# Kernel optimization log

Hardware: AMD Instinct MI355X
Metric: run time of the kernel (lower is better)

The kernel has to match this reference:

```python
import jax, jax.numpy as jnp
import numpy as np

NUM_HEADS = 16


def setup_inputs() -> dict:
    key = jax.random.key(0)
    ks = jax.random.split(key, 7)
    B, S, D = 2, 2048, 1024
    scale = 1.0 / np.sqrt(D)
    return {
        "queries": jax.random.normal(ks[0], (B, S, D), jnp.float32),
        "keys": jax.random.normal(ks[1], (B, S, D), jnp.float32),
        "values": jax.random.normal(ks[2], (B, S, D), jnp.float32),
        "Wq": jax.random.normal(ks[3], (D, D), jnp.float32) * scale,
        "Wk": jax.random.normal(ks[4], (D, D), jnp.float32) * scale,
        "Wv": jax.random.normal(ks[5], (D, D), jnp.float32) * scale,
        "Wo": jax.random.normal(ks[6], (D, D), jnp.float32) * scale,
    }


def _split_heads(x, h):
    # [B, S, D] -> [B, h, S, D/h]
    B, S, D = x.shape
    return x.reshape(B, S, h, D // h).transpose(0, 2, 1, 3)


def reference(queries, keys, values, Wq, Wk, Wv, Wo):
    h = NUM_HEADS
    q = _split_heads(queries @ Wq, h)  # [B, h, S, dh]
    k = _split_heads(keys @ Wk, h)
    v = _split_heads(values @ Wv, h)
    dh = q.shape[-1]
    scores = jnp.einsum("bhqd,bhkd->bhqk", q, k) / jnp.sqrt(jnp.float32(dh))
    attn = jax.nn.softmax(scores, axis=-1)
    y = jnp.einsum("bhqk,bhkd->bhqd", attn, v)  # [B, h, S, dh]
    B, _, S, _ = y.shape
    y = y.transpose(0, 2, 1, 3).reshape(B, S, h * dh)
    return y @ Wo
```

## Files before the change

### kernel.cpp

```cpp
#include <hip/hip_runtime.h>
#include <hip/hip_bf16.h>


typedef __attribute__((ext_vector_type(8))) short bf16x8;
typedef __attribute__((ext_vector_type(4))) float f32x4;
typedef __attribute__((ext_vector_type(16))) float f32x16;
typedef __attribute__((ext_vector_type(4))) unsigned int u32x4;

#define QSCALE 0.18033688011112042f

__device__ __forceinline__ unsigned short f2b(float f) {
    unsigned int u = __float_as_uint(f);
    u += 0x7FFFu + ((u >> 16) & 1u);
    return (unsigned short)(u >> 16);
}

__device__ __forceinline__ unsigned cvt_pk_bf16(float lo, float hi) {
    unsigned r;
    asm("v_cvt_pk_bf16_f32 %0, %1, %2" : "=v"(r) : "v"(lo), "v"(hi));
    return r;
}

__device__ __forceinline__ void gld_lds16(const void* g, void* l) {
    __builtin_amdgcn_global_load_lds(
        (const __attribute__((address_space(1))) unsigned int*)g,
        (__attribute__((address_space(3))) unsigned int*)l, 16, 0, 0);
}

__global__ __launch_bounds__(256) void f32_to_bf16_3(
    const float* __restrict__ i0, const float* __restrict__ i1, const float* __restrict__ i2,
    unsigned short* __restrict__ o0, unsigned short* __restrict__ o1, unsigned short* __restrict__ o2)
{
    const int z = blockIdx.y;
    const float* in = z == 0 ? i0 : (z == 1 ? i1 : i2);
    unsigned short* out = z == 0 ? o0 : (z == 1 ? o1 : o2);
    int i = blockIdx.x * 256 + threadIdx.x;
    float4 v = ((const float4*)in)[i];
    ushort4 o;
    o.x = f2b(v.x); o.y = f2b(v.y); o.z = f2b(v.z); o.w = f2b(v.w);
    ((ushort4*)out)[i] = o;
}

__global__ __launch_bounds__(256) void transpose_w4(
    const float* __restrict__ W0, const float* __restrict__ W1,
    const float* __restrict__ W2, const float* __restrict__ W3,
    unsigned short* __restrict__ O0, unsigned short* __restrict__ O1,
    unsigned short* __restrict__ O2, unsigned short* __restrict__ O3)
{
    __shared__ unsigned short tile[32][33];
    const int z = blockIdx.z;
    const float* in = z == 0 ? W0 : z == 1 ? W1 : z == 2 ? W2 : W3;
    unsigned short* out = z == 0 ? O0 : z == 1 ? O1 : z == 2 ? O2 : O3;
    const int c0 = blockIdx.x * 32, r0 = blockIdx.y * 32;
    const int tx = threadIdx.x, ty = threadIdx.y;
#pragma unroll
    for (int i = 0; i < 4; ++i)
        tile[ty + i * 8][tx] = f2b(in[(size_t)(r0 + ty + i * 8) * 1024 + c0 + tx]);
    __syncthreads();
#pragma unroll
    for (int i = 0; i < 4; ++i)
        out[(size_t)(c0 + ty + i * 8) * 1024 + r0 + tx] = tile[tx][ty + i * 8];
}

__device__ __forceinline__ void vpack_store(unsigned short* Vp, int gr, int gc,
                                            const f32x4& a)
{
    int bq = gr >> 11, kvg = gr & 2047, kvt = kvg >> 6;
    int h = gc >> 6, d = gc & 63;
    size_t img = ((size_t)(bq * 16 + h) * 32 + kvt) * 4096;
    int kvb = kvg & 63;
    int T = kvb >> 5, g = (kvb >> 3) & 3, hib = (kvb >> 2) & 1;
    int kstep = 2 * T + (g >> 1);
    int dt = d >> 5, ln31 = d & 31;
    size_t addr = img + dt * 2048 + kstep * 512 + hib * 256 + ln31 * 8 + (g & 1) * 4;
    uint2 w;
    w.x = cvt_pk_bf16(a[0], a[1]);
    w.y = cvt_pk_bf16(a[2], a[3]);
    *(uint2*)(Vp + addr) = w;
}

__device__ __forceinline__ void kpack_store(unsigned short* Kp, int gr0, int gc,
                                            const f32x4& a)
{
    int bq = gr0 >> 11, kvg = gr0 & 2047, kvt = kvg >> 6;
    int h = gc >> 6, d = gc & 63;
    size_t img = ((size_t)(bq * 16 + h) * 32 + kvt) * 4096;
    int ks = d >> 4, hib = (d >> 3) & 1, i = d & 7;
    int kvb = kvg & 63, T = kvb >> 5;
    size_t base = img + T * 2048 + ks * 512 + hib * 256 + i;
#pragma unroll
    for (int r = 0; r < 4; ++r)
        Kp[base + ((kvb & 31) + r) * 8] = f2b(a[r]);
}

__device__ __forceinline__ int lds_fragaddr(int slot, int mat, int half, int row,
                                            int ks, int lg)
{
    int c8s = lg ^ ((row >> 1) & 3);
    return slot * 32768 + mat * 16384 + half * 8192 +
           (((row >> 4) * 2 + ks) * 512) + (row & 15) * 32 + c8s * 8;
}

__global__ __launch_bounds__(512, 2) void gemm256(
    const unsigned short* __restrict__ A0, const unsigned short* __restrict__ A1,
    const unsigned short* __restrict__ A2,
    const unsigned short* __restrict__ B0, const unsigned short* __restrict__ B1,
    const unsigned short* __restrict__ B2,
    unsigned short* __restrict__ Cq,
    unsigned short* __restrict__ Ck,
    unsigned short* __restrict__ Cv)
{
    __shared__ unsigned short lds[65536];
    const int tid = threadIdx.x;
    const int wid = tid >> 6, ln = tid & 15, lg = (tid & 63) >> 4;
    const int wr = wid >> 2, wc = wid & 3;
    const int z = blockIdx.z;
    const unsigned short* A = (z == 0) ? A0 : (z == 1) ? A1 : A2;
    const unsigned short* Bt = (z == 0) ? B0 : (z == 1) ? B1 : B2;
    const int m0 = blockIdx.y * 256, n0 = blockIdx.x * 256;

    f32x4 acc[8][4];
#pragma unroll
    for (int m = 0; m < 8; ++m)
#pragma unroll
        for (int n = 0; n < 4; ++n) acc[m][n] = {};

    const unsigned short* srcA[2][2];
    const unsigned short* srcB[2][2];
#pragma unroll
    for (int j = 0; j < 2; ++j) {
        const int ci = tid + j * 512;
        const int s = ci >> 6, r16 = (ci >> 2) & 15, c8 = ci & 3;
        const int c8s = c8 ^ ((r16 >> 1) & 3);
        const int rih = (s >> 1) * 16 + r16;
        const int colc = (s & 1) * 4 + c8s;
#pragma unroll
        for (int half = 0; half < 2; ++half) {
            srcA[j][half] = A + (size_t)(m0 + half * 128 + rih) * 1024 + colc * 8;
            srcB[j][half] = Bt + (size_t)(n0 + half * 128 + rih) * 1024 + colc * 8;
        }
    }

    auto stage = [&](int slot, int k0) {
#pragma unroll
        for (int j = 0; j < 2; ++j) {
            const int ci = tid + j * 512;
#pragma unroll
            for (int half = 0; half < 2; ++half) {
                gld_lds16(srcA[j][half] + k0,
                          &lds[slot * 32768 + half * 8192 + ci * 8]);
                gld_lds16(srcB[j][half] + k0,
                          &lds[slot * 32768 + 16384 + half * 8192 + ci * 8]);
            }
        }
    };

    stage(0, 0);
    __syncthreads();

    for (int t = 0; t < 16; ++t) {
        const int slot = t & 1;
        if (t < 15) stage(slot ^ 1, (t + 1) * 64);

#pragma unroll
        for (int qd = 0; qd < 4; ++qd) {
            const int mh = qd >> 1, nh = qd & 1;
            bf16x8 af[4][2], bfr[2][2];
#pragma unroll
            for (int mm = 0; mm < 4; ++mm)
#pragma unroll
                for (int ks = 0; ks < 2; ++ks)
                    af[mm][ks] = *(const bf16x8*)&lds[
                        lds_fragaddr(slot, 0, wr, (mh * 4 + mm) * 16 + ln, ks, lg)];
#pragma unroll
            for (int nn = 0; nn < 2; ++nn)
#pragma unroll
                for (int ks = 0; ks < 2; ++ks)
                    bfr[nn][ks] = *(const bf16x8*)&lds[
                        lds_fragaddr(slot, 1, wc >> 1,
                                     (wc & 1) * 64 + (nh * 2 + nn) * 16 + ln, ks, lg)];
            __builtin_amdgcn_s_setprio(1);
#pragma unroll
            for (int mm = 0; mm < 4; ++mm)
#pragma unroll
                for (int nn = 0; nn < 2; ++nn)
#pragma unroll
                    for (int ks = 0; ks < 2; ++ks)
                        acc[mh * 4 + mm][nh * 2 + nn] =
                            __builtin_amdgcn_mfma_f32_16x16x32_bf16(
                                af[mm][ks], bfr[nn][ks],
                                acc[mh * 4 + mm][nh * 2 + nn], 0, 0, 0);
            __builtin_amdgcn_s_setprio(0);
        }
        __syncthreads();
    }

#pragma unroll
    for (int m = 0; m < 8; ++m)
#pragma unroll
        for (int n = 0; n < 4; ++n) {
            const int gr = m0 + wr * 128 + m * 16 + lg * 4;
            const int gc = n0 + wc * 64 + n * 16 + ln;
            if (z == 0) {
#pragma unroll
                for (int r = 0; r < 4; ++r)
                    Cq[(size_t)(gr + r) * 1024 + gc] = f2b(acc[m][n][r] * QSCALE);
            } else if (z == 1) {
                kpack_store(Ck, gr, gc, acc[m][n]);
            } else {
                vpack_store(Cv, gr, gc, acc[m][n]);
            }
        }
}

template <int BN, int MODE>
__global__ __launch_bounds__(256) void gemm_bt(
    const unsigned short* __restrict__ A0,
    const unsigned short* __restrict__ B0,
    void* __restrict__ Cq)
{
    constexpr int K = 1024, N = 1024;
    constexpr int NB = BN / 32;
    __shared__ unsigned short lds_a[2][128 * 32];
    __shared__ unsigned short lds_b[2][BN * 32];
    const int tid = threadIdx.x;
    const int wid = tid >> 6, ln = tid & 15, lg = (tid & 63) >> 4;
    const unsigned short* A = A0;
    const unsigned short* Bt = B0;
    const int m0 = blockIdx.y * 128, n0 = blockIdx.x * BN;
    const int wr = wid >> 1, wc = wid & 1;

    f32x4 acc[4][NB];
#pragma unroll
    for (int m = 0; m < 4; ++m)
#pragma unroll
        for (int n = 0; n < NB; ++n) acc[m][n] = {};

    const unsigned short* ga = A + (size_t)(m0 + (tid >> 2)) * K + (tid & 3) * 8;
    const unsigned short* gb = Bt + (size_t)(n0 + (tid >> 2)) * K + (tid & 3) * 8;

    auto stage = [&](int buf, int k0) {
        gld_lds16(ga + k0, &lds_a[buf][wid * 512]);
        gld_lds16(ga + k0 + 64 * K, &lds_a[buf][wid * 512 + 2048]);
        gld_lds16(gb + k0, &lds_b[buf][wid * 512]);
        if constexpr (BN == 128) gld_lds16(gb + k0 + 64 * K, &lds_b[buf][wid * 512 + 2048]);
    };

    stage(0, 0);
    __syncthreads();

    for (int k0 = 0; k0 < K; k0 += 32) {
        const int buf = (k0 >> 5) & 1;
        if (k0 + 32 < K) stage(buf ^ 1, k0 + 32);

        bf16x8 af[4], bfr[NB];
#pragma unroll
        for (int m = 0; m < 4; ++m)
            af[m] = *(const bf16x8*)&lds_a[buf][(wr * 64 + m * 16 + ln) * 32 + lg * 8];
#pragma unroll
        for (int n = 0; n < NB; ++n)
            bfr[n] = *(const bf16x8*)&lds_b[buf][(wc * (BN / 2) + n * 16 + ln) * 32 + lg * 8];
#pragma unroll
        for (int m = 0; m < 4; ++m)
#pragma unroll
            for (int n = 0; n < NB; ++n)
                acc[m][n] = __builtin_amdgcn_mfma_f32_16x16x32_bf16(af[m], bfr[n], acc[m][n], 0, 0, 0);
        __syncthreads();
    }

    const int gcb = n0 + wc * (BN / 2) + ln;
    const int grb = m0 + wr * 64 + lg * 4;
    float* C = (float*)Cq;
#pragma unroll
    for (int m = 0; m < 4; ++m)
#pragma unroll
        for (int n = 0; n < NB; ++n)
#pragma unroll
            for (int r = 0; r < 4; ++r)
                C[(size_t)(grb + m * 16 + r) * N + gcb + n * 16] = acc[m][n][r];
}

__global__ __launch_bounds__(128) void attn_kernel(
    const unsigned short* __restrict__ Qp,
    const unsigned short* __restrict__ Kpack,
    const unsigned short* __restrict__ Vpack,
    unsigned short* __restrict__ Y)
{
    __shared__ unsigned short lds_k[2][4096];
    __shared__ unsigned short lds_v[2][4096];
    const int tid = threadIdx.x;
    const int wid = tid >> 6, lane = tid & 63;
    const int q31 = lane & 31, hi = lane >> 5;

    const int logical = (blockIdx.x & 7) * 128 + (blockIdx.x >> 3);
    const int bx = logical & 31, bh = logical >> 5;
    const int b = bh >> 4, h = bh & 15;
    const int tok0 = b * 2048;
    const int qw = bx * 64 + wid * 32;

    const unsigned short* qrow = Qp + (size_t)(tok0 + qw + q31) * 1024 + h * 64 + hi * 8;
    bf16x8 qf[4];
#pragma unroll
    for (int ks = 0; ks < 4; ++ks) qf[ks] = *(const bf16x8*)(qrow + ks * 16);

    const unsigned short* gk = Kpack + (size_t)bh * (32 * 4096);
    const unsigned short* gv = Vpack + (size_t)bh * (32 * 4096);

    float l_run = 0.f;
    f32x16 o[2] = {{}, {}};

    auto stage = [&](int buf, int kvt) {
#pragma unroll
        for (int j = 0; j < 4; ++j) {
            int seg = wid * 4 + j;
            gld_lds16(gk + (size_t)kvt * 4096 + seg * 512 + lane * 8, &lds_k[buf][seg * 512]);
            gld_lds16(gv + (size_t)kvt * 4096 + seg * 512 + lane * 8, &lds_v[buf][seg * 512]);
        }
    };

    stage(0, 0);
    __syncthreads();

    for (int kvt = 0; kvt < 32; ++kvt) {
        const int buf = kvt & 1;
        if (kvt < 31) stage(buf ^ 1, kvt + 1);

        f32x16 st[2];
#pragma unroll
        for (int T = 0; T < 2; ++T) {
            f32x16 zacc = {};
#pragma unroll
            for (int ks = 0; ks < 4; ++ks) {
                bf16x8 ka = *(const bf16x8*)&lds_k[buf][T * 2048 + ks * 512 + lane * 8];
                zacc = __builtin_amdgcn_mfma_f32_32x32x16_bf16(ka, qf[ks], zacc, 0, 0, 0);
            }
            st[T] = zacc;
        }

        float rs = 0.f;
        unsigned pk[2][8];
#pragma unroll
        for (int T = 0; T < 2; ++T)
#pragma unroll
            for (int g = 0; g < 4; ++g) {
                float p0 = __builtin_amdgcn_exp2f(st[T][g * 4 + 0]);
                float p1 = __builtin_amdgcn_exp2f(st[T][g * 4 + 1]);
                float p2 = __builtin_amdgcn_exp2f(st[T][g * 4 + 2]);
                float p3 = __builtin_amdgcn_exp2f(st[T][g * 4 + 3]);
                rs += (p0 + p1) + (p2 + p3);
                pk[T][g * 2 + 0] = cvt_pk_bf16(p0, p1);
                pk[T][g * 2 + 1] = cvt_pk_bf16(p2, p3);
            }
        rs += __shfl_xor(rs, 32);
        l_run += rs;

#pragma unroll
        for (int dt = 0; dt < 2; ++dt)
#pragma unroll
            for (int kstep = 0; kstep < 4; ++kstep) {
                bf16x8 va = *(const bf16x8*)&lds_v[buf][dt * 2048 + kstep * 512 + lane * 8];
                u32x4 w = {pk[kstep >> 1][4 * (kstep & 1) + 0], pk[kstep >> 1][4 * (kstep & 1) + 1],
                           pk[kstep >> 1][4 * (kstep & 1) + 2], pk[kstep >> 1][4 * (kstep & 1) + 3]};
                o[dt] = __builtin_amdgcn_mfma_f32_32x32x16_bf16(
                    va, __builtin_bit_cast(bf16x8, w), o[dt], 0, 0, 0);
            }
        __syncthreads();
    }

    const float inv = __builtin_amdgcn_rcpf(l_run);
    unsigned short* yout = Y + (size_t)(tok0 + qw + q31) * 1024 + h * 64 + hi * 4;
#pragma unroll
    for (int dt = 0; dt < 2; ++dt)
#pragma unroll
        for (int g = 0; g < 4; ++g) {
            uint2 w;
            w.x = cvt_pk_bf16(o[dt][g * 4 + 0] * inv, o[dt][g * 4 + 1] * inv);
            w.y = cvt_pk_bf16(o[dt][g * 4 + 2] * inv, o[dt][g * 4 + 3] * inv);
            *(uint2*)(yout + dt * 32 + g * 8) = w;
        }
}

extern "C" void kernel_launch(void* const* d_in, const int* in_sizes, int n_in,
                              void* d_out, int out_size, void* d_ws, size_t ws_size,
                              hipStream_t stream)
{
    const float* q_f = (const float*)d_in[0];
    const float* k_f = (const float*)d_in[1];
    const float* v_f = (const float*)d_in[2];
    const float* Wq  = (const float*)d_in[3];
    const float* Wk  = (const float*)d_in[4];
    const float* Wv  = (const float*)d_in[5];
    const float* Wo  = (const float*)d_in[6];
    float* out = (float*)d_out;

    const size_t X = (size_t)4096 * 1024;
    const size_t W = (size_t)1024 * 1024;
    unsigned short* ws  = (unsigned short*)d_ws;
    unsigned short* qb  = ws;
    unsigned short* kb  = qb + X;
    unsigned short* vb  = kb + X;
    unsigned short* wqt = vb + X;
    unsigned short* wkt = wqt + W;
    unsigned short* wvt = wkt + W;
    unsigned short* wot = wvt + W;
    unsigned short* Qp  = wot + W;
    unsigned short* Kpk = Qp + X;
    unsigned short* Vpk = Kpk + X;
    unsigned short* Yb  = Vpk + X;

    f32_to_bf16_3<<<dim3(4096, 3), 256, 0, stream>>>(q_f, k_f, v_f, qb, kb, vb);
    transpose_w4<<<dim3(32, 32, 4), dim3(32, 8), 0, stream>>>(Wq, Wk, Wv, Wo,
                                                              wqt, wkt, wvt, wot);

    gemm256<<<dim3(4, 16, 3), 512, 0, stream>>>(qb, kb, vb, wqt, wkt, wvt,
                                                Qp, Kpk, Vpk);

    attn_kernel<<<1024, 128, 0, stream>>>(Qp, Kpk, Vpk, Yb);

    gemm_bt<64, 0><<<dim3(16, 32), 256, 0, stream>>>(Yb, wot, out);
}
```

Baseline: 231.0 us.

## Software-pipeline attention PV with next QK and enlarge attention and output tiles

The attention kernel now runs 4 waves per block, each covering 128 query rows, and launches half as many blocks, so every staged K/V tile is shared by more waves. The loop is software-pipelined: the PV MFMAs for the previous KV tile are issued after the current QK^T, using double-buffered V fragments and packed probabilities, which overlaps the exp/convert work with matrix ops. The row-sum shuffle is moved out of the loop to run once at the end. The output-projection GEMM also switches to a 128-wide tile, which raises register pressure and lowers block count in exchange for more reuse.

```diff
diff --git a/kernel.cpp b/kernel.cpp
--- a/kernel.cpp
+++ b/kernel.cpp
@@ -280,7 +280,7 @@
                 C[(size_t)(grb + m * 16 + r) * N + gcb + n * 16] = acc[m][n][r];
 }
 
-__global__ __launch_bounds__(128) void attn_kernel(
+__global__ __launch_bounds__(256) void attn_kernel(
     const unsigned short* __restrict__ Qp,
     const unsigned short* __restrict__ Kpack,
     const unsigned short* __restrict__ Vpack,
@@ -292,11 +292,11 @@
     const int wid = tid >> 6, lane = tid & 63;
     const int q31 = lane & 31, hi = lane >> 5;
 
-    const int logical = (blockIdx.x & 7) * 128 + (blockIdx.x >> 3);
-    const int bx = logical & 31, bh = logical >> 5;
+    const int logical = (blockIdx.x & 7) * 64 + (blockIdx.x >> 3);
+    const int bx = logical & 15, bh = logical >> 4;
     const int b = bh >> 4, h = bh & 15;
     const int tok0 = b * 2048;
-    const int qw = bx * 64 + wid * 32;
+    const int qw = bx * 128 + wid * 32;
 
     const unsigned short* qrow = Qp + (size_t)(tok0 + qw + q31) * 1024 + h * 64 + hi * 8;
     bf16x8 qf[4];
@@ -311,34 +311,51 @@
 
     auto stage = [&](int buf, int kvt) {
 #pragma unroll
-        for (int j = 0; j < 4; ++j) {
-            int seg = wid * 4 + j;
+        for (int j = 0; j < 2; ++j) {
+            int seg = wid * 2 + j;
             gld_lds16(gk + (size_t)kvt * 4096 + seg * 512 + lane * 8, &lds_k[buf][seg * 512]);
             gld_lds16(gv + (size_t)kvt * 4096 + seg * 512 + lane * 8, &lds_v[buf][seg * 512]);
         }
     };
 
-    stage(0, 0);
-    __syncthreads();
-
-    for (int kvt = 0; kvt < 32; ++kvt) {
+    auto pv = [&](const bf16x8 (&vaP)[8], const unsigned (&pkP)[16]) {
+#pragma unroll
+        for (int dt = 0; dt < 2; ++dt)
+#pragma unroll
+            for (int kstep = 0; kstep < 4; ++kstep) {
+                u32x4 w = {pkP[(kstep >> 1) * 8 + 4 * (kstep & 1) + 0],
+                           pkP[(kstep >> 1) * 8 + 4 * (kstep & 1) + 1],
+                           pkP[(kstep >> 1) * 8 + 4 * (kstep & 1) + 2],
+                           pkP[(kstep >> 1) * 8 + 4 * (kstep & 1) + 3]};
+                o[dt] = __builtin_amdgcn_mfma_f32_32x32x16_bf16(
+                    vaP[dt * 4 + kstep], __builtin_bit_cast(bf16x8, w), o[dt], 0, 0, 0);
+            }
+    };
+
+    auto iter = [&](int kvt, const bf16x8 (&vaP)[8], const unsigned (&pkP)[16],
+                    bf16x8 (&vaC)[8], unsigned (&pkC)[16]) {
         const int buf = kvt & 1;
         if (kvt < 31) stage(buf ^ 1, kvt + 1);
 
         f32x16 st[2];
 #pragma unroll
         for (int T = 0; T < 2; ++T) {
-            f32x16 zacc = {};
+            f32x16 z = {};
 #pragma unroll
             for (int ks = 0; ks < 4; ++ks) {
                 bf16x8 ka = *(const bf16x8*)&lds_k[buf][T * 2048 + ks * 512 + lane * 8];
-                zacc = __builtin_amdgcn_mfma_f32_32x32x16_bf16(ka, qf[ks], zacc, 0, 0, 0);
+                z = __builtin_amdgcn_mfma_f32_32x32x16_bf16(ka, qf[ks], z, 0, 0, 0);
             }
-            st[T] = zacc;
-        }
+            st[T] = z;
+        }
+
+#pragma unroll
+        for (int f = 0; f < 8; ++f)
+            vaC[f] = *(const bf16x8*)&lds_v[buf][f * 512 + lane * 8];
+
+        pv(vaP, pkP);
 
         float rs = 0.f;
-        unsigned pk[2][8];
 #pragma unroll
         for (int T = 0; T < 2; ++T)
 #pragma unroll
@@ -348,25 +365,31 @@
                 float p2 = __builtin_amdgcn_exp2f(st[T][g * 4 + 2]);
                 float p3 = __builtin_amdgcn_exp2f(st[T][g * 4 + 3]);
                 rs += (p0 + p1) + (p2 + p3);
-                pk[T][g * 2 + 0] = cvt_pk_bf16(p0, p1);
-                pk[T][g * 2 + 1] = cvt_pk_bf16(p2, p3);
+                pkC[T * 8 + g * 2 + 0] = cvt_pk_bf16(p0, p1);
+                pkC[T * 8 + g * 2 + 1] = cvt_pk_bf16(p2, p3);
             }
-        rs += __shfl_xor(rs, 32);
         l_run += rs;
-
-#pragma unroll
-        for (int dt = 0; dt < 2; ++dt)
-#pragma unroll
-            for (int kstep = 0; kstep < 4; ++kstep) {
-                bf16x8 va = *(const bf16x8*)&lds_v[buf][dt * 2048 + kstep * 512 + lane * 8];
-                u32x4 w = {pk[kstep >> 1][4 * (kstep & 1) + 0], pk[kstep >> 1][4 * (kstep & 1) + 1],
-                           pk[kstep >> 1][4 * (kstep & 1) + 2], pk[kstep >> 1][4 * (kstep & 1) + 3]};
-                o[dt] = __builtin_amdgcn_mfma_f32_32x32x16_bf16(
-                    va, __builtin_bit_cast(bf16x8, w), o[dt], 0, 0, 0);
-            }
         __syncthreads();
+    };
+
+    stage(0, 0);
+    __syncthreads();
+
+    bf16x8 vaA[8], vaB[8];
+    unsigned pkA[16], pkB[16];
+    const bf16x8 zb = {};
+#pragma unroll
+    for (int f = 0; f < 8; ++f) vaA[f] = zb;
+#pragma unroll
+    for (int f = 0; f < 16; ++f) pkA[f] = 0;
+
+    for (int t2 = 0; t2 < 16; ++t2) {
+        iter(2 * t2,     vaA, pkA, vaB, pkB);
+        iter(2 * t2 + 1, vaB, pkB, vaA, pkA);
     }
-
+    pv(vaA, pkA);
+
+    l_run += __shfl_xor(l_run, 32);
     const float inv = __builtin_amdgcn_rcpf(l_run);
     unsigned short* yout = Y + (size_t)(tok0 + qw + q31) * 1024 + h * 64 + hi * 4;
 #pragma unroll
@@ -415,7 +438,7 @@
     gemm256<<<dim3(4, 16, 3), 512, 0, stream>>>(qb, kb, vb, wqt, wkt, wvt,
                                                 Qp, Kpk, Vpk);
 
-    attn_kernel<<<1024, 128, 0, stream>>>(Qp, Kpk, Vpk, Yb);
-
-    gemm_bt<64, 0><<<dim3(16, 32), 256, 0, stream>>>(Yb, wot, out);
-}
+    attn_kernel<<<512, 256, 0, stream>>>(Qp, Kpk, Vpk, Yb);
+
+    gemm_bt<128, 0><<<dim3(8, 32), 256, 0, stream>>>(Yb, wot, out);
+}
```

Result: faster. 207.8 us (-10.0%).
